# Performance work log

Measured on AMD Instinct MI355X. Metric: run time of the kernel, lower is better.

## Reference

```python
import jax, jax.numpy as jnp
import numpy as np

NS, NA = 50000, 50000
ES, EA = 1000000, 500000
XD, UD, HD, MH = 8, 8, 64, 64


def _mlp_params(key, d_in, d_h, d_out):
    ks = jax.random.split(key, 3)
    s = 0.05
    return (jax.random.normal(ks[0], (d_in, d_h), jnp.float32) * s, jnp.zeros((d_h,), jnp.float32),
            jax.random.normal(ks[1], (d_h, d_h), jnp.float32) * s, jnp.zeros((d_h,), jnp.float32),
            jax.random.normal(ks[2], (d_h, d_out), jnp.float32) * s, jnp.zeros((d_out,), jnp.float32))


def _mlp(z, w1, b1, w2, b2, w3, b3):
    z = jnp.tanh(z @ w1 + b1)
    z = jnp.tanh(z @ w2 + b2)
    return z @ w3 + b3


def setup_inputs() -> dict:
    key = jax.random.key(0)
    ks = jax.random.split(key, 12)
    inp = {
        'pos_state': jax.random.uniform(ks[0], (NS, 2), jnp.float32),
        'pos_action': jax.random.uniform(ks[1], (NA, 2), jnp.float32),
        'h': jax.random.normal(ks[2], (NS, HD), jnp.float32),
        'x': jax.random.normal(ks[3], (NS, XD), jnp.float32),
        'u': jax.random.normal(ks[4], (NA, UD), jnp.float32),
        'a2s_src': jax.random.randint(ks[5], (EA,), 0, NA, jnp.int32),
        'a2s_dst': jax.random.randint(ks[6], (EA,), 0, NS, jnp.int32),
        'a2s_dis': jax.random.uniform(ks[7], (EA, 1), jnp.float32),
        's2s_src': jax.random.randint(ks[8], (ES,), 0, NS, jnp.int32),
        's2s_dst': jax.random.randint(ks[9], (ES,), 0, NS, jnp.int32),
        's2s_dis': jax.random.uniform(ks[10], (ES, 1), jnp.float32),
    }
    pk = jax.random.split(ks[11], 3)
    u2h = _mlp_params(pk[0], 2 * 2 + 1 + UD, MH, HD)
    x2h = _mlp_params(pk[1], 2 * 2 + 1 + XD + HD, MH, HD)
    upd = _mlp_params(pk[2], 2 + 3 * HD + XD, MH, HD)
    for pref, p in (('u2h', u2h), ('x2h', x2h), ('upd', upd)):
        for i, (w, b) in enumerate(zip(p[0::2], p[1::2]), 1):
            inp[f'{pref}_w{i}'] = w
            inp[f'{pref}_b{i}'] = b
    return inp


def reference(pos_state, pos_action, h, x, u,
              a2s_src, a2s_dst, a2s_dis, s2s_src, s2s_dst, s2s_dis,
              u2h_w1, u2h_b1, u2h_w2, u2h_b2, u2h_w3, u2h_b3,
              x2h_w1, x2h_b1, x2h_w2, x2h_b2, x2h_w3, x2h_b3,
              upd_w1, upd_b1, upd_w2, upd_b2, upd_w3, upd_b3):
    ns = pos_state.shape[0]
    # a2s: gather action src / state dst, per-edge MLP, sum into dst state nodes
    msg_u_in = jnp.concatenate([pos_action[a2s_src], pos_state[a2s_dst], a2s_dis, u[a2s_src]], axis=-1)
    msg_u = _mlp(msg_u_in, u2h_w1, u2h_b1, u2h_w2, u2h_b2, u2h_w3, u2h_b3)  # [EA, HD]
    sum_u = jax.ops.segment_sum(msg_u, a2s_dst, num_segments=ns)
    # s2s: gather state src/dst, per-edge MLP, mean into dst state nodes
    msg_x_in = jnp.concatenate([pos_state[s2s_src], pos_state[s2s_dst], s2s_dis, x[s2s_src], h[s2s_src]], axis=-1)
    msg_x = _mlp(msg_x_in, x2h_w1, x2h_b1, x2h_w2, x2h_b2, x2h_w3, x2h_b3)  # [ES, HD]
    sum_x = jax.ops.segment_sum(msg_x, s2s_dst, num_segments=ns)
    deg = jax.ops.segment_sum(jnp.ones((s2s_dst.shape[0],), jnp.float32), s2s_dst, num_segments=ns)
    mean_x = sum_x / jnp.maximum(deg, 1.0)[:, None]  # DGL mean: 0 for zero in-degree
    # node update MLP
    upd_in = jnp.concatenate([pos_state, h, sum_u, mean_x, x], axis=-1)
    return _mlp(upd_in, upd_w1, upd_b1, upd_w2, upd_b2, upd_w3, upd_b3)
```

## Files before the change

kernel.cpp:

```cpp
#include <hip/hip_runtime.h>
#include <hip/hip_bf16.h>


typedef __attribute__((ext_vector_type(8))) short short8;
typedef __attribute__((ext_vector_type(4))) float f32x4;

#define MFMA(a, b, c) __builtin_amdgcn_mfma_f32_16x16x32_bf16(a, b, c, 0, 0, 0)

union FU { short8 v; unsigned int d[4]; unsigned short us[8]; };

__device__ __forceinline__ unsigned short f2bf(float f) {
    unsigned u = __float_as_uint(f);
    u += 0x7fffu + ((u >> 16) & 1u);
    return (unsigned short)(u >> 16);
}
__device__ __forceinline__ unsigned int pack2(float a, float b) {
    return (unsigned int)f2bf(a) | ((unsigned int)f2bf(b) << 16);
}
__device__ __forceinline__ unsigned int pk2(float a, float b) {
    float2 t; t.x = a; t.y = b;
    union { __hip_bfloat162 h; unsigned int u; } c;
    c.h = __float22bfloat162_rn(t);
    return c.u;
}
__device__ __forceinline__ float tanh_fast(float xv) {
    float t = __builtin_amdgcn_exp2f(xv * 2.8853900817779268f);
    return 1.0f - 2.0f * __builtin_amdgcn_rcpf(t + 1.0f);
}

template <typename KM>
__device__ void build_gfrags(const float* __restrict__ w, unsigned short* dst,
                             int nchunks, int gtid, int gstr, KM km) {
    int total = nchunks * 4 * 64;
    for (int f = gtid; f < total; f += gstr) {
        int lv = f & 63, nt = (f >> 6) & 3, c = f >> 8;
        int n = nt * 16 + (lv & 15);
        int kb = c * 32 + ((lv >> 4) << 3);
        unsigned short* o = dst + f * 8;
        #pragma unroll
        for (int j = 0; j < 8; ++j) {
            int sk = km(kb + j);
            o[j] = (sk >= 0) ? f2bf(w[sk * 64 + n]) : (unsigned short)0;
        }
    }
}

#define PERM_KM [](int k) -> int { return (k >> 2) + 16 * (k & 3); }

__global__ __launch_bounds__(256) void build_wtab(
    const float* __restrict__ s_w1, const float* __restrict__ s_w2, const float* __restrict__ s_w3,
    const float* __restrict__ a_w1, const float* __restrict__ a_w2, const float* __restrict__ a_w3,
    const float* __restrict__ u_w1, const float* __restrict__ u_w2, const float* __restrict__ u_w3,
    unsigned short* __restrict__ ts, unsigned short* __restrict__ ta,
    unsigned short* __restrict__ tu)
{
    int gtid = blockIdx.x * 256 + threadIdx.x;
    int gstr = gridDim.x * 256;
    build_gfrags(s_w1, ts, 3, gtid, gstr, [](int k) -> int {
        if (k < 2)   return k;
        if (k < 74)  return k + 3;
        if (k < 80)  return -2;
        if (k < 82)  return k - 78;
        if (k == 82) return 4;
        return -2; });
    build_gfrags(s_w2, ts + 3 * 2048, 2, gtid, gstr, PERM_KM);
    build_gfrags(s_w3, ts + 5 * 2048, 2, gtid, gstr, PERM_KM);
    build_gfrags(a_w1, ta, 1, gtid, gstr, [](int k) -> int {
        if (k < 2)   return k;
        if (k < 10)  return k + 3;
        if (k < 16)  return -2;
        if (k < 18)  return k - 14;
        if (k == 18) return 4;
        return -2; });
    build_gfrags(a_w2, ta + 1 * 2048, 2, gtid, gstr, PERM_KM);
    build_gfrags(a_w3, ta + 3 * 2048, 2, gtid, gstr, PERM_KM);
    build_gfrags(u_w1, tu, 7, gtid, gstr, [](int k) -> int {
        return (k < 202) ? k : -2; });
    build_gfrags(u_w2, tu + 7 * 2048, 2, gtid, gstr, PERM_KM);
    build_gfrags(u_w3, tu + 9 * 2048, 2, gtid, gstr, PERM_KM);
}

#define ZTRANS(Zw, accv)                                                       \
    _Pragma("unroll")                                                          \
    for (int r = 0; r < 4; ++r) {                                              \
        uint2 pv;                                                              \
        pv.x = pk2(tanh_fast(accv[0][r]), tanh_fast(accv[1][r]));              \
        pv.y = pk2(tanh_fast(accv[2][r]), tanh_fast(accv[3][r]));              \
        *(uint2*)((Zw) + ((q << 2) + r) * 72 + (m16 << 2)) = pv;               \
    }

__global__ __launch_bounds__(256) void prep1(
    const float* __restrict__ ps, const float* __restrict__ pa,
    const float* __restrict__ h, const float* __restrict__ x,
    const float* __restrict__ u,
    const int* __restrict__ s2s_dst, const int* __restrict__ a2s_dst,
    unsigned short* __restrict__ s_row, unsigned short* __restrict__ a_row,
    int* __restrict__ cnt_s, int* __restrict__ rank_s,
    int* __restrict__ cnt_a, int* __restrict__ rank_a,
    int NS, int NA, int ES, int EA)
{
    int R0 = NS * 80, R1 = R0 + NA * 16, R2 = R1 + ES, R3 = R2 + EA;
    for (int i = blockIdx.x * 256 + threadIdx.x; i < R3; i += gridDim.x * 256) {
        if (i < R0) {
            int n = i / 80, k = i - n * 80;
            float v = (k < 2) ? ps[n * 2 + k] : (k < 10) ? x[n * 8 + k - 2]
                    : (k < 74) ? h[n * 64 + k - 10] : 0.f;
            s_row[i] = f2bf(v);
        } else if (i < R1) {
            int j = i - R0; int a = j / 16, k = j - a * 16;
            float v = (k < 2) ? pa[a * 2 + k] : (k < 10) ? u[a * 8 + k - 2] : 0.f;
            a_row[j] = f2bf(v);
        } else if (i < R2) {
            int e = i - R1;
            rank_s[e] = atomicAdd(&cnt_s[s2s_dst[e]], 1);
        } else {
            int e = i - R2;
            rank_a[e] = atomicAdd(&cnt_a[a2s_dst[e]], 1);
        }
    }
}

#define SCAN_CHUNK 1024

__global__ __launch_bounds__(256) void scan_a(const int* __restrict__ cnt,
                                              int* __restrict__ bsum, int N2)
{
    __shared__ int red[256];
    int t = threadIdx.x;
    int base = blockIdx.x * SCAN_CHUNK + t * 4;
    int s = 0;
    #pragma unroll
    for (int j = 0; j < 4; ++j) { int i = base + j; if (i < N2) s += cnt[i]; }
    red[t] = s; __syncthreads();
    for (int d = 128; d > 0; d >>= 1) {
        if (t < d) red[t] += red[t + d];
        __syncthreads();
    }
    if (t == 0) bsum[blockIdx.x] = red[0];
}

__global__ __launch_bounds__(128) void scan_b(int* __restrict__ bsum, int NB)
{
    __shared__ int part[128];
    int t = threadIdx.x;
    int v = (t < NB) ? bsum[t] : 0;
    part[t] = v; __syncthreads();
    for (int d = 1; d < 128; d <<= 1) {
        int w = (t >= d) ? part[t - d] : 0;
        __syncthreads();
        part[t] += w;
        __syncthreads();
    }
    if (t < NB) bsum[t] = part[t] - v;
}

__global__ __launch_bounds__(256) void scan_c(const int* __restrict__ cnt,
                                              const int* __restrict__ bsum,
                                              int* __restrict__ off,
                                              int N2, int NS, int ES)
{
    __shared__ int part[256];
    int t = threadIdx.x;
    int base = blockIdx.x * SCAN_CHUNK + t * 4;
    int c[4]; int s = 0;
    #pragma unroll
    for (int j = 0; j < 4; ++j) { int i = base + j; c[j] = (i < N2) ? cnt[i] : 0; s += c[j]; }
    part[t] = s; __syncthreads();
    for (int d = 1; d < 256; d <<= 1) {
        int w = (t >= d) ? part[t - d] : 0;
        __syncthreads();
        part[t] += w;
        __syncthreads();
    }
    int run = bsum[blockIdx.x] + part[t] - s;
    #pragma unroll
    for (int j = 0; j < 4; ++j) {
        int i = base + j;
        if (i < N2) off[i] = run - ((i >= NS) ? ES : 0);
        run += c[j];
    }
}

__global__ __launch_bounds__(256) void scatter_sort2(
    const int* __restrict__ srcS, const int* __restrict__ dstS,
    const int* __restrict__ rankS, const int* __restrict__ offS,
    const float* __restrict__ disS,
    const int* __restrict__ srcA, const int* __restrict__ dstA,
    const int* __restrict__ rankA, const int* __restrict__ offA,
    const float* __restrict__ disA,
    const float* __restrict__ ps,
    int* __restrict__ ssrcS, int* __restrict__ sdstS, unsigned short* __restrict__ spadS,
    int* __restrict__ ssrcA, int* __restrict__ sdstA, unsigned short* __restrict__ spadA,
    int ES, int EA)
{
    int tot = ES + EA;
    for (int i = blockIdx.x * 256 + threadIdx.x; i < tot; i += gridDim.x * 256) {
        if (i < ES) {
            int d = dstS[i];
            int pos = offS[d] + rankS[i];
            ssrcS[pos] = srcS[i];
            sdstS[pos] = d;
            uint2 p;
            p.x = pack2(ps[d * 2], ps[d * 2 + 1]);
            p.y = (unsigned)f2bf(disS[i]) | (0x3F80u << 16);
            *(uint2*)(spadS + (size_t)pos * 4) = p;
        } else {
            int e = i - ES;
            int d = dstA[e];
            int pos = offA[d] + rankA[e];
            ssrcA[pos] = srcA[e];
            sdstA[pos] = d;
            uint2 p;
            p.x = pack2(ps[d * 2], ps[d * 2 + 1]);
            p.y = (unsigned)f2bf(disA[e]) | (0x3F80u << 16);
            *(uint2*)(spadA + (size_t)pos * 4) = p;
        }
    }
}

__global__ __launch_bounds__(256) void s2s_mfma(
    const unsigned short* __restrict__ s_row,
    const int* __restrict__ ssrc, const int* __restrict__ sdst,
    const unsigned short* __restrict__ spad,
    const unsigned short* __restrict__ wtab,
    const float* __restrict__ b1, const float* __restrict__ b2,
    const float* __restrict__ b3,
    float* __restrict__ sum_x, int E)
{
    __shared__ __align__(16) unsigned short WT[7 * 2048];
    __shared__ __align__(16) unsigned short Z[4][16 * 72];

    int tid = threadIdx.x;
    for (int i = tid * 8; i < 7 * 2048; i += 256 * 8)
        *(short8*)(WT + i) = *(const short8*)(wtab + i);
    __syncthreads();

    const unsigned short* W1 = WT;
    const unsigned short* W2 = WT + 3 * 2048;
    const unsigned short* W3 = WT + 5 * 2048;

    int wid = tid >> 6, lane = tid & 63, m16 = lane & 15, q = lane >> 4;
    unsigned short* Zw = Z[wid];

    float bb1[4], bb2[4], bb3[4];
    #pragma unroll
    for (int nt = 0; nt < 4; ++nt) {
        bb1[nt] = b1[nt * 16 + m16];
        bb2[nt] = b2[nt * 16 + m16];
        bb3[nt] = b3[nt * 16 + m16];
    }

    int T = E >> 5;
    for (int t = blockIdx.x * 4 + wid; t < T; t += gridDim.x * 4) {
        int p0 = t * 32;
        int sp0 = p0 + ((m16 >> 2) << 3) + (m16 & 3);
        int sp1 = sp0 + 4;
        int s0 = ssrc[sp0], s1 = ssrc[sp1];
        int pb = p0 + (q << 3);
        int4 dq0 = *(const int4*)(sdst + pb);
        int4 dq1 = *(const int4*)(sdst + pb + 4);
        int dseq[8] = {dq0.x, dq0.y, dq0.z, dq0.w, dq1.x, dq1.y, dq1.z, dq1.w};

        FU Lb[2][3]; uint2 ep[2];
        const unsigned short* rA = s_row + (size_t)s0 * 80;
        const unsigned short* rB = s_row + (size_t)s1 * 80;
        #pragma unroll
        for (int c = 0; c < 3; ++c) {
            Lb[0][c].v = *(const short8*)(rA + c * 32 + q * 8);
            Lb[1][c].v = *(const short8*)(rB + c * 32 + q * 8);
        }
        ep[0] = *(const uint2*)(spad + (size_t)sp0 * 4);
        ep[1] = *(const uint2*)(spad + (size_t)sp1 * 4);
        #pragma unroll
        for (int mt = 0; mt < 2; ++mt) {
            FU f = Lb[mt][2];
            f.d[0] = q < 2 ? f.d[0] : (q == 2 ? ep[mt].x : 0u);
            f.d[1] = q < 2 ? f.d[1] : (q == 2 ? ep[mt].y : 0u);
            f.d[2] = q < 2 ? f.d[2] : 0u;
            f.d[3] = q < 2 ? f.d[3] : 0u;
            Lb[mt][2] = f;
        }

        f32x4 acc1[2][4];
        #pragma unroll
        for (int mt = 0; mt < 2; ++mt)
            #pragma unroll
            for (int nt = 0; nt < 4; ++nt)
                acc1[mt][nt] = (f32x4){bb1[nt], bb1[nt], bb1[nt], bb1[nt]};
        #pragma unroll
        for (int c = 0; c < 3; ++c)
            #pragma unroll
            for (int nt = 0; nt < 4; ++nt) {
                short8 wf = *(const short8*)(W1 + ((c * 4 + nt) * 64 + lane) * 8);
                acc1[0][nt] = MFMA(Lb[0][c].v, wf, acc1[0][nt]);
                acc1[1][nt] = MFMA(Lb[1][c].v, wf, acc1[1][nt]);
            }

        f32x4 a3[2][4];
        #pragma unroll
        for (int mt = 0; mt < 2; ++mt) {
            ZTRANS(Zw, acc1[mt])
            FU A2[2];
            A2[0].v = *(const short8*)(Zw + m16 * 72 + 0 * 32 + q * 8);
            A2[1].v = *(const short8*)(Zw + m16 * 72 + 1 * 32 + q * 8);

            f32x4 a2[4];
            #pragma unroll
            for (int nt = 0; nt < 4; ++nt) {
                a2[nt] = (f32x4){bb2[nt], bb2[nt], bb2[nt], bb2[nt]};
                short8 w0 = *(const short8*)(W2 + ((0 * 4 + nt) * 64 + lane) * 8);
                short8 w1f = *(const short8*)(W2 + ((1 * 4 + nt) * 64 + lane) * 8);
                a2[nt] = MFMA(A2[0].v, w0, a2[nt]);
                a2[nt] = MFMA(A2[1].v, w1f, a2[nt]);
            }

            ZTRANS(Zw, a2)
            FU A3[2];
            A3[0].v = *(const short8*)(Zw + m16 * 72 + 0 * 32 + q * 8);
            A3[1].v = *(const short8*)(Zw + m16 * 72 + 1 * 32 + q * 8);

            #pragma unroll
            for (int nt = 0; nt < 4; ++nt) {
                a3[mt][nt] = (f32x4){bb3[nt], bb3[nt], bb3[nt], bb3[nt]};
                short8 w0 = *(const short8*)(W3 + ((0 * 4 + nt) * 64 + lane) * 8);
                short8 w1f = *(const short8*)(W3 + ((1 * 4 + nt) * 64 + lane) * 8);
                a3[mt][nt] = MFMA(A3[0].v, w0, a3[mt][nt]);
                a3[mt][nt] = MFMA(A3[1].v, w1f, a3[mt][nt]);
            }
        }

        #pragma unroll
        for (int j = 0; j < 8; ++j) {
            int mt = j >> 2, r = j & 3;
            bool merge = (j < 7) && (dseq[j] == dseq[j + 1]);
            if (merge) {
                int mt2 = (j + 1) >> 2, r2 = (j + 1) & 3;
                #pragma unroll
                for (int nt = 0; nt < 4; ++nt) a3[mt2][nt][r2] += a3[mt][nt][r];
            } else {
                float* pbase = sum_x + (size_t)dseq[j] * 64 + m16;
                #pragma unroll
                for (int nt = 0; nt < 4; ++nt)
                    unsafeAtomicAdd(pbase + nt * 16, a3[mt][nt][r]);
            }
        }
    }
}

__global__ __launch_bounds__(256) void a2s_mfma(
    const unsigned short* __restrict__ a_row,
    const int* __restrict__ ssrc, const int* __restrict__ sdst,
    const unsigned short* __restrict__ spad,
    const unsigned short* __restrict__ wtab,
    const float* __restrict__ b1, const float* __restrict__ b2,
    const float* __restrict__ b3,
    float* __restrict__ sum_u, int E)
{
    __shared__ __align__(16) unsigned short WT[5 * 2048];
    __shared__ __align__(16) unsigned short Z[4][16 * 72];

    int tid = threadIdx.x;
    for (int i = tid * 8; i < 5 * 2048; i += 256 * 8)
        *(short8*)(WT + i) = *(const short8*)(wtab + i);
    __syncthreads();

    const unsigned short* W1 = WT;
    const unsigned short* W2 = WT + 1 * 2048;
    const unsigned short* W3 = WT + 3 * 2048;

    int wid = tid >> 6, lane = tid & 63, m16 = lane & 15, q = lane >> 4;
    unsigned short* Zw = Z[wid];

    float bb1[4], bb2[4], bb3[4];
    #pragma unroll
    for (int nt = 0; nt < 4; ++nt) {
        bb1[nt] = b1[nt * 16 + m16];
        bb2[nt] = b2[nt * 16 + m16];
        bb3[nt] = b3[nt * 16 + m16];
    }

    int T = E >> 5;
    for (int t = blockIdx.x * 4 + wid; t < T; t += gridDim.x * 4) {
        int p0 = t * 32;
        int sp0 = p0 + ((m16 >> 2) << 3) + (m16 & 3);
        int sp1 = sp0 + 4;
        int s0 = ssrc[sp0], s1 = ssrc[sp1];
        int pb = p0 + (q << 3);
        int4 dq0 = *(const int4*)(sdst + pb);
        int4 dq1 = *(const int4*)(sdst + pb + 4);
        int dseq[8] = {dq0.x, dq0.y, dq0.z, dq0.w, dq1.x, dq1.y, dq1.z, dq1.w};

        FU Lb[2]; uint2 ep[2];
        Lb[0].v = *(const short8*)(a_row + (size_t)s0 * 16 + q * 8);
        Lb[1].v = *(const short8*)(a_row + (size_t)s1 * 16 + q * 8);
        ep[0] = *(const uint2*)(spad + (size_t)sp0 * 4);
        ep[1] = *(const uint2*)(spad + (size_t)sp1 * 4);
        #pragma unroll
        for (int mt = 0; mt < 2; ++mt) {
            FU f = Lb[mt];
            f.d[0] = q < 2 ? f.d[0] : (q == 2 ? ep[mt].x : 0u);
            f.d[1] = q < 2 ? f.d[1] : (q == 2 ? ep[mt].y : 0u);
            f.d[2] = q < 2 ? f.d[2] : 0u;
            f.d[3] = q < 2 ? f.d[3] : 0u;
            Lb[mt] = f;
        }

        f32x4 acc1[2][4];
        #pragma unroll
        for (int mt = 0; mt < 2; ++mt)
            #pragma unroll
            for (int nt = 0; nt < 4; ++nt)
                acc1[mt][nt] = (f32x4){bb1[nt], bb1[nt], bb1[nt], bb1[nt]};
        #pragma unroll
        for (int nt = 0; nt < 4; ++nt) {
            short8 wf = *(const short8*)(W1 + (nt * 64 + lane) * 8);
            acc1[0][nt] = MFMA(Lb[0].v, wf, acc1[0][nt]);
            acc1[1][nt] = MFMA(Lb[1].v, wf, acc1[1][nt]);
        }

        f32x4 a3[2][4];
        #pragma unroll
        for (int mt = 0; mt < 2; ++mt) {
            ZTRANS(Zw, acc1[mt])
            FU A2[2];
            A2[0].v = *(const short8*)(Zw + m16 * 72 + 0 * 32 + q * 8);
            A2[1].v = *(const short8*)(Zw + m16 * 72 + 1 * 32 + q * 8);

            f32x4 a2[4];
            #pragma unroll
            for (int nt = 0; nt < 4; ++nt) {
                a2[nt] = (f32x4){bb2[nt], bb2[nt], bb2[nt], bb2[nt]};
                short8 w0 = *(const short8*)(W2 + ((0 * 4 + nt) * 64 + lane) * 8);
                short8 w1f = *(const short8*)(W2 + ((1 * 4 + nt) * 64 + lane) * 8);
                a2[nt] = MFMA(A2[0].v, w0, a2[nt]);
                a2[nt] = MFMA(A2[1].v, w1f, a2[nt]);
            }

            ZTRANS(Zw, a2)
            FU A3[2];
            A3[0].v = *(const short8*)(Zw + m16 * 72 + 0 * 32 + q * 8);
            A3[1].v = *(const short8*)(Zw + m16 * 72 + 1 * 32 + q * 8);

            #pragma unroll
            for (int nt = 0; nt < 4; ++nt) {
                a3[mt][nt] = (f32x4){bb3[nt], bb3[nt], bb3[nt], bb3[nt]};
                short8 w0 = *(const short8*)(W3 + ((0 * 4 + nt) * 64 + lane) * 8);
                short8 w1f = *(const short8*)(W3 + ((1 * 4 + nt) * 64 + lane) * 8);
                a3[mt][nt] = MFMA(A3[0].v, w0, a3[mt][nt]);
                a3[mt][nt] = MFMA(A3[1].v, w1f, a3[mt][nt]);
            }
        }

        #pragma unroll
        for (int j = 0; j < 8; ++j) {
            int mt = j >> 2, r = j & 3;
            bool merge = (j < 7) && (dseq[j] == dseq[j + 1]);
            if (merge) {
                int mt2 = (j + 1) >> 2, r2 = (j + 1) & 3;
                #pragma unroll
                for (int nt = 0; nt < 4; ++nt) a3[mt2][nt][r2] += a3[mt][nt][r];
            } else {
                float* pbase = sum_u + (size_t)dseq[j] * 64 + m16;
                #pragma unroll
                for (int nt = 0; nt < 4; ++nt)
                    unsafeAtomicAdd(pbase + nt * 16, a3[mt][nt][r]);
            }
        }
    }
}

__global__ __launch_bounds__(256) void prep2(
    const float* __restrict__ ps, const float* __restrict__ h,
    const float* __restrict__ x,
    const float* __restrict__ su, const float* __restrict__ sx,
    const int* __restrict__ cnt_s, unsigned short* __restrict__ u_row, int NS)
{
    int n = blockIdx.x;
    int k = threadIdx.x;
    if (k >= 224) return;
    float v;
    if (k < 2)        v = ps[n * 2 + k];
    else if (k < 66)  v = h[n * 64 + k - 2];
    else if (k < 130) v = su[n * 64 + k - 66];
    else if (k < 194) v = sx[n * 64 + k - 130] * (1.0f / fmaxf((float)cnt_s[n], 1.0f));
    else if (k < 202) v = x[n * 8 + k - 194];
    else              v = 0.f;
    u_row[(size_t)n * 224 + k] = f2bf(v);
}

__global__ __launch_bounds__(256) void upd_mfma(
    const unsigned short* __restrict__ u_row,
    const unsigned short* __restrict__ wtab,
    const float* __restrict__ b1, const float* __restrict__ b2,
    const float* __restrict__ b3,
    float* __restrict__ out, int NS)
{
    __shared__ __align__(16) unsigned short WT[11 * 2048];
    __shared__ __align__(16) unsigned short Z[4][16 * 72];

    int tid = threadIdx.x;
    for (int i = tid * 8; i < 11 * 2048; i += 256 * 8)
        *(short8*)(WT + i) = *(const short8*)(wtab + i);
    __syncthreads();

    const unsigned short* W1 = WT;
    const unsigned short* W2 = WT + 7 * 2048;
    const unsigned short* W3 = WT + 9 * 2048;

    int wid = tid >> 6, lane = tid & 63, m16 = lane & 15, q = lane >> 4;
    unsigned short* Zw = Z[wid];

    float bb1[4], bb2[4], bb3[4];
    #pragma unroll
    for (int nt = 0; nt < 4; ++nt) {
        bb1[nt] = b1[nt * 16 + m16];
        bb2[nt] = b2[nt * 16 + m16];
        bb3[nt] = b3[nt * 16 + m16];
    }

    int T = NS >> 4;
    for (int t = blockIdx.x * 4 + wid; t < T; t += gridDim.x * 4) {
        int n0 = t * 16;
        const unsigned short* row = u_row + (size_t)(n0 + m16) * 224;

        f32x4 acc1[4];
        #pragma unroll
        for (int nt = 0; nt < 4; ++nt)
            acc1[nt] = (f32x4){bb1[nt], bb1[nt], bb1[nt], bb1[nt]};
        #pragma unroll
        for (int c = 0; c < 7; ++c) {
            short8 afrag = *(const short8*)(row + c * 32 + q * 8);
            #pragma unroll
            for (int nt = 0; nt < 4; ++nt) {
                short8 wf = *(const short8*)(W1 + ((c * 4 + nt) * 64 + lane) * 8);
                acc1[nt] = MFMA(afrag, wf, acc1[nt]);
            }
        }

        ZTRANS(Zw, acc1)
        FU A2[2];
        A2[0].v = *(const short8*)(Zw + m16 * 72 + 0 * 32 + q * 8);
        A2[1].v = *(const short8*)(Zw + m16 * 72 + 1 * 32 + q * 8);

        f32x4 a2[4];
        #pragma unroll
        for (int nt = 0; nt < 4; ++nt) {
            a2[nt] = (f32x4){bb2[nt], bb2[nt], bb2[nt], bb2[nt]};
            short8 w0 = *(const short8*)(W2 + ((0 * 4 + nt) * 64 + lane) * 8);
            short8 w1f = *(const short8*)(W2 + ((1 * 4 + nt) * 64 + lane) * 8);
            a2[nt] = MFMA(A2[0].v, w0, a2[nt]);
            a2[nt] = MFMA(A2[1].v, w1f, a2[nt]);
        }

        ZTRANS(Zw, a2)
        FU A3[2];
        A3[0].v = *(const short8*)(Zw + m16 * 72 + 0 * 32 + q * 8);
        A3[1].v = *(const short8*)(Zw + m16 * 72 + 1 * 32 + q * 8);

        f32x4 a3[4];
        #pragma unroll
        for (int nt = 0; nt < 4; ++nt) {
            a3[nt] = (f32x4){bb3[nt], bb3[nt], bb3[nt], bb3[nt]};
            short8 w0 = *(const short8*)(W3 + ((0 * 4 + nt) * 64 + lane) * 8);
            short8 w1f = *(const short8*)(W3 + ((1 * 4 + nt) * 64 + lane) * 8);
            a3[nt] = MFMA(A3[0].v, w0, a3[nt]);
            a3[nt] = MFMA(A3[1].v, w1f, a3[nt]);
        }

        #pragma unroll
        for (int nt = 0; nt < 4; ++nt)
            #pragma unroll
            for (int r = 0; r < 4; ++r)
                out[(size_t)(n0 + (q << 2) + r) * 64 + nt * 16 + m16] = a3[nt][r];
    }
}

extern "C" void kernel_launch(void* const* d_in, const int* in_sizes, int n_in,
                              void* d_out, int out_size, void* d_ws, size_t ws_size,
                              hipStream_t stream) {
    const float* pos_state  = (const float*)d_in[0];
    const float* pos_action = (const float*)d_in[1];
    const float* h          = (const float*)d_in[2];
    const float* x          = (const float*)d_in[3];
    const float* u          = (const float*)d_in[4];
    const int*   a2s_src    = (const int*)d_in[5];
    const int*   a2s_dst    = (const int*)d_in[6];
    const float* a2s_dis    = (const float*)d_in[7];
    const int*   s2s_src    = (const int*)d_in[8];
    const int*   s2s_dst    = (const int*)d_in[9];
    const float* s2s_dis    = (const float*)d_in[10];
    const float* u2h_w1 = (const float*)d_in[11]; const float* u2h_b1 = (const float*)d_in[12];
    const float* u2h_w2 = (const float*)d_in[13]; const float* u2h_b2 = (const float*)d_in[14];
    const float* u2h_w3 = (const float*)d_in[15]; const float* u2h_b3 = (const float*)d_in[16];
    const float* x2h_w1 = (const float*)d_in[17]; const float* x2h_b1 = (const float*)d_in[18];
    const float* x2h_w2 = (const float*)d_in[19]; const float* x2h_b2 = (const float*)d_in[20];
    const float* x2h_w3 = (const float*)d_in[21]; const float* x2h_b3 = (const float*)d_in[22];
    const float* upd_w1 = (const float*)d_in[23]; const float* upd_b1 = (const float*)d_in[24];
    const float* upd_w2 = (const float*)d_in[25]; const float* upd_b2 = (const float*)d_in[26];
    const float* upd_w3 = (const float*)d_in[27]; const float* upd_b3 = (const float*)d_in[28];

    int NS = in_sizes[0] / 2;
    int NA = in_sizes[1] / 2;
    int EA = in_sizes[5];
    int ES = in_sizes[8];
    int N2 = 2 * NS;
    int NB = (N2 + SCAN_CHUNK - 1) / SCAN_CHUNK;

    char* p = (char*)d_ws;
    int*   cnt2  = (int*)p;            p += (size_t)N2 * 4;
    float* sum_u = (float*)p;          p += (size_t)NS * 64 * 4;
    float* sum_x = (float*)p;          p += (size_t)NS * 64 * 4;
    size_t zbytes = (size_t)(p - (char*)d_ws);
    unsigned short* u_row = (unsigned short*)p;
    int*   off2   = (int*)p;           p += (size_t)N2 * 4;
    int*   rank_s = (int*)p;           p += (size_t)ES * 4;
    int*   rank_a = (int*)p;           p += (size_t)EA * 4;
    int*   ssrc_s = (int*)p;           p += (size_t)ES * 4;
    int*   sdst_s = (int*)p;           p += (size_t)ES * 4;
    unsigned short* spad_s = (unsigned short*)p; p += (size_t)ES * 8;
    int*   ssrc_a = (int*)p;           p += (size_t)EA * 4;
    int*   sdst_a = (int*)p;           p += (size_t)EA * 4;
    unsigned short* spad_a = (unsigned short*)p; p += (size_t)EA * 8;
    unsigned short* s_row  = (unsigned short*)p; p += (size_t)NS * 80 * 2;
    unsigned short* a_row  = (unsigned short*)p; p += (size_t)NA * 16 * 2;
    int*   bsum   = (int*)p;           p += 128 * 4;
    unsigned short* wtab_s = (unsigned short*)p; p += 7 * 2048 * 2;
    unsigned short* wtab_a = (unsigned short*)p; p += 5 * 2048 * 2;
    unsigned short* wtab_u = (unsigned short*)p; p += 11 * 2048 * 2;
    (void)ws_size;

    int* cnt_s = cnt2;
    int* cnt_a = cnt2 + NS;
    int* off_s = off2;
    int* off_a = off2 + NS;

    hipMemsetAsync(d_ws, 0, zbytes, stream);

    build_wtab<<<24, 256, 0, stream>>>(x2h_w1, x2h_w2, x2h_w3,
                                       u2h_w1, u2h_w2, u2h_w3,
                                       upd_w1, upd_w2, upd_w3,
                                       wtab_s, wtab_a, wtab_u);
    prep1<<<2048, 256, 0, stream>>>(pos_state, pos_action, h, x, u,
                                    s2s_dst, a2s_dst,
                                    s_row, a_row,
                                    cnt_s, rank_s, cnt_a, rank_a,
                                    NS, NA, ES, EA);
    scan_a<<<NB, 256, 0, stream>>>(cnt2, bsum, N2);
    scan_b<<<1, 128, 0, stream>>>(bsum, NB);
    scan_c<<<NB, 256, 0, stream>>>(cnt2, bsum, off2, N2, NS, ES);
    scatter_sort2<<<1024, 256, 0, stream>>>(s2s_src, s2s_dst, rank_s, off_s, s2s_dis,
                                            a2s_src, a2s_dst, rank_a, off_a, a2s_dis,
                                            pos_state,
                                            ssrc_s, sdst_s, spad_s,
                                            ssrc_a, sdst_a, spad_a, ES, EA);
    a2s_mfma<<<1024, 256, 0, stream>>>(a_row, ssrc_a, sdst_a, spad_a, wtab_a,
                                       u2h_b1, u2h_b2, u2h_b3, sum_u, EA);
    s2s_mfma<<<1024, 256, 0, stream>>>(s_row, ssrc_s, sdst_s, spad_s, wtab_s,
                                       x2h_b1, x2h_b2, x2h_b3, sum_x, ES);
    prep2<<<NS, 256, 0, stream>>>(pos_state, h, x, sum_u, sum_x, cnt_s, u_row, NS);
    upd_mfma<<<784, 256, 0, stream>>>(u_row, wtab_u,
                                      upd_b1, upd_b2, upd_b3,
                                      (float*)d_out, NS);
}
```

Measured before the change: 508.8 us.

## Fuse weight prep into prep1, merge edge kernels, fold prep2 into upd

Folds the weight-fragment build into extra blocks of prep1, merges the a2s and s2s edge MLP kernels into one launch split by block index, and removes prep2 by having upd_mfma read h, sums and x directly in fp32 and convert to bf16 in registers. The scatter stage now stores the raw fp32 distance instead of a packed bf16 pad, and the edge kernel gathers dst positions itself. Fewer launches and one less full intermediate buffer round-trip, at the cost of extra gathers inside the edge kernel and a reordered upd weight layout.

```diff
diff --git a/kernel.cpp b/kernel.cpp
--- a/kernel.cpp
+++ b/kernel.cpp
@@ -13,9 +13,6 @@
     unsigned u = __float_as_uint(f);
     u += 0x7fffu + ((u >> 16) & 1u);
     return (unsigned short)(u >> 16);
-}
-__device__ __forceinline__ unsigned int pack2(float a, float b) {
-    return (unsigned int)f2bf(a) | ((unsigned int)f2bf(b) << 16);
 }
 __device__ __forceinline__ unsigned int pk2(float a, float b) {
     float2 t; t.x = a; t.y = b;
@@ -47,39 +44,6 @@
 
 #define PERM_KM [](int k) -> int { return (k >> 2) + 16 * (k & 3); }
 
-__global__ __launch_bounds__(256) void build_wtab(
-    const float* __restrict__ s_w1, const float* __restrict__ s_w2, const float* __restrict__ s_w3,
-    const float* __restrict__ a_w1, const float* __restrict__ a_w2, const float* __restrict__ a_w3,
-    const float* __restrict__ u_w1, const float* __restrict__ u_w2, const float* __restrict__ u_w3,
-    unsigned short* __restrict__ ts, unsigned short* __restrict__ ta,
-    unsigned short* __restrict__ tu)
-{
-    int gtid = blockIdx.x * 256 + threadIdx.x;
-    int gstr = gridDim.x * 256;
-    build_gfrags(s_w1, ts, 3, gtid, gstr, [](int k) -> int {
-        if (k < 2)   return k;
-        if (k < 74)  return k + 3;
-        if (k < 80)  return -2;
-        if (k < 82)  return k - 78;
-        if (k == 82) return 4;
-        return -2; });
-    build_gfrags(s_w2, ts + 3 * 2048, 2, gtid, gstr, PERM_KM);
-    build_gfrags(s_w3, ts + 5 * 2048, 2, gtid, gstr, PERM_KM);
-    build_gfrags(a_w1, ta, 1, gtid, gstr, [](int k) -> int {
-        if (k < 2)   return k;
-        if (k < 10)  return k + 3;
-        if (k < 16)  return -2;
-        if (k < 18)  return k - 14;
-        if (k == 18) return 4;
-        return -2; });
-    build_gfrags(a_w2, ta + 1 * 2048, 2, gtid, gstr, PERM_KM);
-    build_gfrags(a_w3, ta + 3 * 2048, 2, gtid, gstr, PERM_KM);
-    build_gfrags(u_w1, tu, 7, gtid, gstr, [](int k) -> int {
-        return (k < 202) ? k : -2; });
-    build_gfrags(u_w2, tu + 7 * 2048, 2, gtid, gstr, PERM_KM);
-    build_gfrags(u_w3, tu + 9 * 2048, 2, gtid, gstr, PERM_KM);
-}
-
 #define ZTRANS(Zw, accv)                                                       \
     _Pragma("unroll")                                                          \
     for (int r = 0; r < 4; ++r) {                                              \
@@ -97,10 +61,47 @@
     unsigned short* __restrict__ s_row, unsigned short* __restrict__ a_row,
     int* __restrict__ cnt_s, int* __restrict__ rank_s,
     int* __restrict__ cnt_a, int* __restrict__ rank_a,
-    int NS, int NA, int ES, int EA)
-{
+    const float* __restrict__ s_w1, const float* __restrict__ s_w2, const float* __restrict__ s_w3,
+    const float* __restrict__ a_w1, const float* __restrict__ a_w2, const float* __restrict__ a_w3,
+    const float* __restrict__ u_w1, const float* __restrict__ u_w2, const float* __restrict__ u_w3,
+    unsigned short* __restrict__ ts, unsigned short* __restrict__ ta,
+    unsigned short* __restrict__ tu,
+    int NS, int NA, int ES, int EA, int MAINB)
+{
+    int bid = blockIdx.x;
+    if (bid >= MAINB) {
+        int gtid = (bid - MAINB) * 256 + threadIdx.x;
+        int gstr = (gridDim.x - MAINB) * 256;
+        build_gfrags(s_w1, ts, 3, gtid, gstr, [](int k) -> int {
+            if (k < 2)   return k;
+            if (k < 74)  return k + 3;
+            if (k < 80)  return -2;
+            if (k < 82)  return k - 78;
+            if (k == 82) return 4;
+            return -2; });
+        build_gfrags(s_w2, ts + 3 * 2048, 2, gtid, gstr, PERM_KM);
+        build_gfrags(s_w3, ts + 5 * 2048, 2, gtid, gstr, PERM_KM);
+        build_gfrags(a_w1, ta, 1, gtid, gstr, [](int k) -> int {
+            if (k < 2)   return k;
+            if (k < 10)  return k + 3;
+            if (k < 16)  return -2;
+            if (k < 18)  return k - 14;
+            if (k == 18) return 4;
+            return -2; });
+        build_gfrags(a_w2, ta + 1 * 2048, 2, gtid, gstr, PERM_KM);
+        build_gfrags(a_w3, ta + 3 * 2048, 2, gtid, gstr, PERM_KM);
+        build_gfrags(u_w1, tu, 7, gtid, gstr, [](int k) -> int {
+            if (k < 192) return k + 2;
+            if (k < 194) return k - 192;
+            if (k < 202) return k;
+            return -2; });
+        build_gfrags(u_w2, tu + 7 * 2048, 2, gtid, gstr, PERM_KM);
+        build_gfrags(u_w3, tu + 9 * 2048, 2, gtid, gstr, PERM_KM);
+        return;
+    }
+
     int R0 = NS * 80, R1 = R0 + NA * 16, R2 = R1 + ES, R3 = R2 + EA;
-    for (int i = blockIdx.x * 256 + threadIdx.x; i < R3; i += gridDim.x * 256) {
+    for (int i = bid * 256 + threadIdx.x; i < R3; i += MAINB * 256) {
         if (i < R0) {
             int n = i / 80, k = i - n * 80;
             float v = (k < 2) ? ps[n * 2 + k] : (k < 10) ? x[n * 8 + k - 2]
@@ -188,9 +189,8 @@
     const int* __restrict__ srcA, const int* __restrict__ dstA,
     const int* __restrict__ rankA, const int* __restrict__ offA,
     const float* __restrict__ disA,
-    const float* __restrict__ ps,
-    int* __restrict__ ssrcS, int* __restrict__ sdstS, unsigned short* __restrict__ spadS,
-    int* __restrict__ ssrcA, int* __restrict__ sdstA, unsigned short* __restrict__ spadA,
+    int* __restrict__ ssrcS, int* __restrict__ sdstS, float* __restrict__ sdisS,
+    int* __restrict__ ssrcA, int* __restrict__ sdstA, float* __restrict__ sdisA,
     int ES, int EA)
 {
     int tot = ES + EA;
@@ -200,47 +200,35 @@
             int pos = offS[d] + rankS[i];
             ssrcS[pos] = srcS[i];
             sdstS[pos] = d;
-            uint2 p;
-            p.x = pack2(ps[d * 2], ps[d * 2 + 1]);
-            p.y = (unsigned)f2bf(disS[i]) | (0x3F80u << 16);
-            *(uint2*)(spadS + (size_t)pos * 4) = p;
+            sdisS[pos] = disS[i];
         } else {
             int e = i - ES;
             int d = dstA[e];
             int pos = offA[d] + rankA[e];
             ssrcA[pos] = srcA[e];
             sdstA[pos] = d;
-            uint2 p;
-            p.x = pack2(ps[d * 2], ps[d * 2 + 1]);
-            p.y = (unsigned)f2bf(disA[e]) | (0x3F80u << 16);
-            *(uint2*)(spadA + (size_t)pos * 4) = p;
-        }
-    }
-}
-
-__global__ __launch_bounds__(256) void s2s_mfma(
-    const unsigned short* __restrict__ s_row,
+            sdisA[pos] = disA[e];
+        }
+    }
+}
+
+template <int C1, int RS>
+__device__ __forceinline__ void edge_path(
+    const unsigned short* __restrict__ row_tab,
     const int* __restrict__ ssrc, const int* __restrict__ sdst,
-    const unsigned short* __restrict__ spad,
-    const unsigned short* __restrict__ wtab,
+    const float* __restrict__ sdis, const float* __restrict__ ps,
+    const unsigned short* WT,
     const float* __restrict__ b1, const float* __restrict__ b2,
     const float* __restrict__ b3,
-    float* __restrict__ sum_x, int E)
-{
-    __shared__ __align__(16) unsigned short WT[7 * 2048];
-    __shared__ __align__(16) unsigned short Z[4][16 * 72];
-
-    int tid = threadIdx.x;
-    for (int i = tid * 8; i < 7 * 2048; i += 256 * 8)
-        *(short8*)(WT + i) = *(const short8*)(wtab + i);
-    __syncthreads();
-
+    float* __restrict__ sums, int E, int bid0, int nb, int tid,
+    unsigned short* Zbase)
+{
     const unsigned short* W1 = WT;
-    const unsigned short* W2 = WT + 3 * 2048;
-    const unsigned short* W3 = WT + 5 * 2048;
+    const unsigned short* W2 = WT + C1 * 2048;
+    const unsigned short* W3 = WT + (C1 + 2) * 2048;
 
     int wid = tid >> 6, lane = tid & 63, m16 = lane & 15, q = lane >> 4;
-    unsigned short* Zw = Z[wid];
+    unsigned short* Zw = Zbase + wid * (16 * 72);
 
     float bb1[4], bb2[4], bb3[4];
     #pragma unroll
@@ -251,7 +239,7 @@
     }
 
     int T = E >> 5;
-    for (int t = blockIdx.x * 4 + wid; t < T; t += gridDim.x * 4) {
+    for (int t = bid0 * 4 + wid; t < T; t += nb * 4) {
         int p0 = t * 32;
         int sp0 = p0 + ((m16 >> 2) << 3) + (m16 & 3);
         int sp1 = sp0 + 4;
@@ -261,24 +249,31 @@
         int4 dq1 = *(const int4*)(sdst + pb + 4);
         int dseq[8] = {dq0.x, dq0.y, dq0.z, dq0.w, dq1.x, dq1.y, dq1.z, dq1.w};
 
-        FU Lb[2][3]; uint2 ep[2];
-        const unsigned short* rA = s_row + (size_t)s0 * 80;
-        const unsigned short* rB = s_row + (size_t)s1 * 80;
-        #pragma unroll
-        for (int c = 0; c < 3; ++c) {
-            Lb[0][c].v = *(const short8*)(rA + c * 32 + q * 8);
-            Lb[1][c].v = *(const short8*)(rB + c * 32 + q * 8);
-        }
-        ep[0] = *(const uint2*)(spad + (size_t)sp0 * 4);
-        ep[1] = *(const uint2*)(spad + (size_t)sp1 * 4);
-        #pragma unroll
-        for (int mt = 0; mt < 2; ++mt) {
-            FU f = Lb[mt][2];
-            f.d[0] = q < 2 ? f.d[0] : (q == 2 ? ep[mt].x : 0u);
-            f.d[1] = q < 2 ? f.d[1] : (q == 2 ? ep[mt].y : 0u);
-            f.d[2] = q < 2 ? f.d[2] : 0u;
-            f.d[3] = q < 2 ? f.d[3] : 0u;
-            Lb[mt][2] = f;
+        uint2 ep[2];
+        ep[0].x = 0; ep[0].y = 0; ep[1].x = 0; ep[1].y = 0;
+        if (q == 2) {
+            int dA = sdst[sp0], dB = sdst[sp1];
+            float2 pA = *(const float2*)(ps + 2 * dA);
+            float2 pB = *(const float2*)(ps + 2 * dB);
+            float zA = sdis[sp0], zB = sdis[sp1];
+            ep[0].x = pk2(pA.x, pA.y); ep[0].y = (unsigned)f2bf(zA) | (0x3F80u << 16);
+            ep[1].x = pk2(pB.x, pB.y); ep[1].y = (unsigned)f2bf(zB) | (0x3F80u << 16);
+        }
+
+        FU Lb[2][C1];
+        const unsigned short* rA = row_tab + (size_t)s0 * RS;
+        const unsigned short* rB = row_tab + (size_t)s1 * RS;
+        #pragma unroll
+        for (int c = 0; c < C1; ++c) {
+            int off = c * 32 + q * 8;
+            bool valid = (c < C1 - 1) || (q < 2);
+            if (valid) {
+                Lb[0][c].v = *(const short8*)(rA + off);
+                Lb[1][c].v = *(const short8*)(rB + off);
+            } else {
+                Lb[0][c].d[0] = ep[0].x; Lb[0][c].d[1] = ep[0].y; Lb[0][c].d[2] = 0; Lb[0][c].d[3] = 0;
+                Lb[1][c].d[0] = ep[1].x; Lb[1][c].d[1] = ep[1].y; Lb[1][c].d[2] = 0; Lb[1][c].d[3] = 0;
+            }
         }
 
         f32x4 acc1[2][4];
@@ -288,7 +283,7 @@
             for (int nt = 0; nt < 4; ++nt)
                 acc1[mt][nt] = (f32x4){bb1[nt], bb1[nt], bb1[nt], bb1[nt]};
         #pragma unroll
-        for (int c = 0; c < 3; ++c)
+        for (int c = 0; c < C1; ++c)
             #pragma unroll
             for (int nt = 0; nt < 4; ++nt) {
                 short8 wf = *(const short8*)(W1 + ((c * 4 + nt) * 64 + lane) * 8);
@@ -338,7 +333,7 @@
                 #pragma unroll
                 for (int nt = 0; nt < 4; ++nt) a3[mt2][nt][r2] += a3[mt][nt][r];
             } else {
-                float* pbase = sum_x + (size_t)dseq[j] * 64 + m16;
+                float* pbase = sums + (size_t)dseq[j] * 64 + m16;
                 #pragma unroll
                 for (int nt = 0; nt < 4; ++nt)
                     unsafeAtomicAdd(pbase + nt * 16, a3[mt][nt][r]);
@@ -347,29 +342,60 @@
     }
 }
 
-__global__ __launch_bounds__(256) void a2s_mfma(
-    const unsigned short* __restrict__ a_row,
-    const int* __restrict__ ssrc, const int* __restrict__ sdst,
-    const unsigned short* __restrict__ spad,
+__global__ __launch_bounds__(256) void edges_mfma(
+    const unsigned short* __restrict__ s_row, const unsigned short* __restrict__ a_row,
+    const int* __restrict__ ssS, const int* __restrict__ sdS, const float* __restrict__ szS,
+    const int* __restrict__ ssA, const int* __restrict__ sdA, const float* __restrict__ szA,
+    const unsigned short* __restrict__ wtS, const unsigned short* __restrict__ wtA,
+    const float* __restrict__ sb1, const float* __restrict__ sb2, const float* __restrict__ sb3,
+    const float* __restrict__ ab1, const float* __restrict__ ab2, const float* __restrict__ ab3,
+    const float* __restrict__ ps,
+    float* __restrict__ sum_x, float* __restrict__ sum_u,
+    int ES, int EA, int SPLIT)
+{
+    __shared__ __align__(16) unsigned short WT[7 * 2048];
+    __shared__ __align__(16) unsigned short Z[4][16 * 72];
+
+    int tid = threadIdx.x, bid = blockIdx.x;
+    bool is_s = bid < SPLIT;
+    const unsigned short* wt = is_s ? wtS : wtA;
+    int wtn = is_s ? 7 * 2048 : 5 * 2048;
+    for (int i = tid * 8; i < wtn; i += 256 * 8)
+        *(short8*)(WT + i) = *(const short8*)(wt + i);
+    __syncthreads();
+
+    if (is_s)
+        edge_path<3, 80>(s_row, ssS, sdS, szS, ps, WT, sb1, sb2, sb3,
+                         sum_x, ES, bid, SPLIT, tid, &Z[0][0]);
+    else
+        edge_path<1, 16>(a_row, ssA, sdA, szA, ps, WT, ab1, ab2, ab3,
+                         sum_u, EA, bid - SPLIT, gridDim.x - SPLIT, tid, &Z[0][0]);
+}
+
+__global__ __launch_bounds__(256) void upd_mfma(
+    const float* __restrict__ ps, const float* __restrict__ h,
+    const float* __restrict__ x,
+    const float* __restrict__ su, const float* __restrict__ sx,
+    const int* __restrict__ cnt_s,
     const unsigned short* __restrict__ wtab,
     const float* __restrict__ b1, const float* __restrict__ b2,
     const float* __restrict__ b3,
-    float* __restrict__ sum_u, int E)
-{
-    __shared__ __align__(16) unsigned short WT[5 * 2048];
+    float* __restrict__ out, int NS)
+{
+    __shared__ __align__(16) unsigned short WT[11 * 2048];
     __shared__ __align__(16) unsigned short Z[4][16 * 72];
 
     int tid = threadIdx.x;
-    for (int i = tid * 8; i < 5 * 2048; i += 256 * 8)
+    for (int i = tid * 8; i < 11 * 2048; i += 256 * 8)
         *(short8*)(WT + i) = *(const short8*)(wtab + i);
     __syncthreads();
 
     const unsigned short* W1 = WT;
-    const unsigned short* W2 = WT + 1 * 2048;
-    const unsigned short* W3 = WT + 3 * 2048;
+    const unsigned short* W2 = WT + 7 * 2048;
+    const unsigned short* W3 = WT + 9 * 2048;
 
     int wid = tid >> 6, lane = tid & 63, m16 = lane & 15, q = lane >> 4;
-    unsigned short* Zw = Z[wid];
+    unsigned short* Zw = &Z[wid][0];
 
     float bb1[4], bb2[4], bb3[4];
     #pragma unroll
@@ -379,163 +405,54 @@
         bb3[nt] = b3[nt * 16 + m16];
     }
 
-    int T = E >> 5;
-    for (int t = blockIdx.x * 4 + wid; t < T; t += gridDim.x * 4) {
-        int p0 = t * 32;
-        int sp0 = p0 + ((m16 >> 2) << 3) + (m16 & 3);
-        int sp1 = sp0 + 4;
-        int s0 = ssrc[sp0], s1 = ssrc[sp1];
-        int pb = p0 + (q << 3);
-        int4 dq0 = *(const int4*)(sdst + pb);
-        int4 dq1 = *(const int4*)(sdst + pb + 4);
-        int dseq[8] = {dq0.x, dq0.y, dq0.z, dq0.w, dq1.x, dq1.y, dq1.z, dq1.w};
-
-        FU Lb[2]; uint2 ep[2];
-        Lb[0].v = *(const short8*)(a_row + (size_t)s0 * 16 + q * 8);
-        Lb[1].v = *(const short8*)(a_row + (size_t)s1 * 16 + q * 8);
-        ep[0] = *(const uint2*)(spad + (size_t)sp0 * 4);
-        ep[1] = *(const uint2*)(spad + (size_t)sp1 * 4);
-        #pragma unroll
-        for (int mt = 0; mt < 2; ++mt) {
-            FU f = Lb[mt];
-            f.d[0] = q < 2 ? f.d[0] : (q == 2 ? ep[mt].x : 0u);
-            f.d[1] = q < 2 ? f.d[1] : (q == 2 ? ep[mt].y : 0u);
-            f.d[2] = q < 2 ? f.d[2] : 0u;
-            f.d[3] = q < 2 ? f.d[3] : 0u;
-            Lb[mt] = f;
-        }
-
-        f32x4 acc1[2][4];
-        #pragma unroll
-        for (int mt = 0; mt < 2; ++mt)
-            #pragma unroll
-            for (int nt = 0; nt < 4; ++nt)
-                acc1[mt][nt] = (f32x4){bb1[nt], bb1[nt], bb1[nt], bb1[nt]};
-        #pragma unroll
-        for (int nt = 0; nt < 4; ++nt) {
-            short8 wf = *(const short8*)(W1 + (nt * 64 + lane) * 8);
-            acc1[0][nt] = MFMA(Lb[0].v, wf, acc1[0][nt]);
-            acc1[1][nt] = MFMA(Lb[1].v, wf, acc1[1][nt]);
-        }
-
-        f32x4 a3[2][4];
-        #pragma unroll
-        for (int mt = 0; mt < 2; ++mt) {
-            ZTRANS(Zw, acc1[mt])
-            FU A2[2];
-            A2[0].v = *(const short8*)(Zw + m16 * 72 + 0 * 32 + q * 8);
-            A2[1].v = *(const short8*)(Zw + m16 * 72 + 1 * 32 + q * 8);
-
-            f32x4 a2[4];
-            #pragma unroll
-            for (int nt = 0; nt < 4; ++nt) {
-                a2[nt] = (f32x4){bb2[nt], bb2[nt], bb2[nt], bb2[nt]};
-                short8 w0 = *(const short8*)(W2 + ((0 * 4 + nt) * 64 + lane) * 8);
-                short8 w1f = *(const short8*)(W2 + ((1 * 4 + nt) * 64 + lane) * 8);
-                a2[nt] = MFMA(A2[0].v, w0, a2[nt]);
-                a2[nt] = MFMA(A2[1].v, w1f, a2[nt]);
-            }
-
-            ZTRANS(Zw, a2)
-            FU A3[2];
-            A3[0].v = *(const short8*)(Zw + m16 * 72 + 0 * 32 + q * 8);
-            A3[1].v = *(const short8*)(Zw + m16 * 72 + 1 * 32 + q * 8);
-
-            #pragma unroll
-            for (int nt = 0; nt < 4; ++nt) {
-                a3[mt][nt] = (f32x4){bb3[nt], bb3[nt], bb3[nt], bb3[nt]};
-                short8 w0 = *(const short8*)(W3 + ((0 * 4 + nt) * 64 + lane) * 8);
-                short8 w1f = *(const short8*)(W3 + ((1 * 4 + nt) * 64 + lane) * 8);
-                a3[mt][nt] = MFMA(A3[0].v, w0, a3[mt][nt]);
-                a3[mt][nt] = MFMA(A3[1].v, w1f, a3[mt][nt]);
-            }
-        }
-
-        #pragma unroll
-        for (int j = 0; j < 8; ++j) {
-            int mt = j >> 2, r = j & 3;
-            bool merge = (j < 7) && (dseq[j] == dseq[j + 1]);
-            if (merge) {
-                int mt2 = (j + 1) >> 2, r2 = (j + 1) & 3;
-                #pragma unroll
-                for (int nt = 0; nt < 4; ++nt) a3[mt2][nt][r2] += a3[mt][nt][r];
-            } else {
-                float* pbase = sum_u + (size_t)dseq[j] * 64 + m16;
-                #pragma unroll
-                for (int nt = 0; nt < 4; ++nt)
-                    unsafeAtomicAdd(pbase + nt * 16, a3[mt][nt][r]);
-            }
-        }
-    }
-}
-
-__global__ __launch_bounds__(256) void prep2(
-    const float* __restrict__ ps, const float* __restrict__ h,
-    const float* __restrict__ x,
-    const float* __restrict__ su, const float* __restrict__ sx,
-    const int* __restrict__ cnt_s, unsigned short* __restrict__ u_row, int NS)
-{
-    int n = blockIdx.x;
-    int k = threadIdx.x;
-    if (k >= 224) return;
-    float v;
-    if (k < 2)        v = ps[n * 2 + k];
-    else if (k < 66)  v = h[n * 64 + k - 2];
-    else if (k < 130) v = su[n * 64 + k - 66];
-    else if (k < 194) v = sx[n * 64 + k - 130] * (1.0f / fmaxf((float)cnt_s[n], 1.0f));
-    else if (k < 202) v = x[n * 8 + k - 194];
-    else              v = 0.f;
-    u_row[(size_t)n * 224 + k] = f2bf(v);
-}
-
-__global__ __launch_bounds__(256) void upd_mfma(
-    const unsigned short* __restrict__ u_row,
-    const unsigned short* __restrict__ wtab,
-    const float* __restrict__ b1, const float* __restrict__ b2,
-    const float* __restrict__ b3,
-    float* __restrict__ out, int NS)
-{
-    __shared__ __align__(16) unsigned short WT[11 * 2048];
-    __shared__ __align__(16) unsigned short Z[4][16 * 72];
-
-    int tid = threadIdx.x;
-    for (int i = tid * 8; i < 11 * 2048; i += 256 * 8)
-        *(short8*)(WT + i) = *(const short8*)(wtab + i);
-    __syncthreads();
-
-    const unsigned short* W1 = WT;
-    const unsigned short* W2 = WT + 7 * 2048;
-    const unsigned short* W3 = WT + 9 * 2048;
-
-    int wid = tid >> 6, lane = tid & 63, m16 = lane & 15, q = lane >> 4;
-    unsigned short* Zw = Z[wid];
-
-    float bb1[4], bb2[4], bb3[4];
-    #pragma unroll
-    for (int nt = 0; nt < 4; ++nt) {
-        bb1[nt] = b1[nt * 16 + m16];
-        bb2[nt] = b2[nt * 16 + m16];
-        bb3[nt] = b3[nt * 16 + m16];
-    }
-
     int T = NS >> 4;
     for (int t = blockIdx.x * 4 + wid; t < T; t += gridDim.x * 4) {
         int n0 = t * 16;
-        const unsigned short* row = u_row + (size_t)(n0 + m16) * 224;
+        int n = n0 + m16;
+        float rd = __builtin_amdgcn_rcpf(fmaxf((float)cnt_s[n], 1.0f));
+
+        FU A[7];
+        const float* hp = h + (size_t)n * 64;
+        const float* sup = su + (size_t)n * 64;
+        const float* sxp = sx + (size_t)n * 64;
+        #pragma unroll
+        for (int c = 0; c < 6; ++c) {
+            const float* src = (c < 2) ? hp : (c < 4) ? sup : sxp;
+            int base = (c & 1) * 32 + q * 8;
+            float4 f0 = *(const float4*)(src + base);
+            float4 f1 = *(const float4*)(src + base + 4);
+            if (c >= 4) {
+                f0.x *= rd; f0.y *= rd; f0.z *= rd; f0.w *= rd;
+                f1.x *= rd; f1.y *= rd; f1.z *= rd; f1.w *= rd;
+            }
+            A[c].d[0] = pk2(f0.x, f0.y); A[c].d[1] = pk2(f0.z, f0.w);
+            A[c].d[2] = pk2(f1.x, f1.y); A[c].d[3] = pk2(f1.z, f1.w);
+        }
+        A[6].d[0] = 0; A[6].d[1] = 0; A[6].d[2] = 0; A[6].d[3] = 0;
+        if (q == 0) {
+            float2 pp = *(const float2*)(ps + 2 * n);
+            float4 x0 = *(const float4*)(x + 8 * n);
+            float2 x1 = *(const float2*)(x + 8 * n + 4);
+            A[6].d[0] = pk2(pp.x, pp.y);
+            A[6].d[1] = pk2(x0.x, x0.y);
+            A[6].d[2] = pk2(x0.z, x0.w);
+            A[6].d[3] = pk2(x1.x, x1.y);
+        } else if (q == 1) {
+            float2 x2 = *(const float2*)(x + 8 * n + 6);
+            A[6].d[0] = pk2(x2.x, x2.y);
+        }
 
         f32x4 acc1[4];
         #pragma unroll
         for (int nt = 0; nt < 4; ++nt)
             acc1[nt] = (f32x4){bb1[nt], bb1[nt], bb1[nt], bb1[nt]};
         #pragma unroll
-        for (int c = 0; c < 7; ++c) {
-            short8 afrag = *(const short8*)(row + c * 32 + q * 8);
+        for (int c = 0; c < 7; ++c)
             #pragma unroll
             for (int nt = 0; nt < 4; ++nt) {
                 short8 wf = *(const short8*)(W1 + ((c * 4 + nt) * 64 + lane) * 8);
-                acc1[nt] = MFMA(afrag, wf, acc1[nt]);
-            }
-        }
+                acc1[nt] = MFMA(A[c].v, wf, acc1[nt]);
+            }
 
         ZTRANS(Zw, acc1)
         FU A2[2];
@@ -611,16 +528,15 @@
     float* sum_u = (float*)p;          p += (size_t)NS * 64 * 4;
     float* sum_x = (float*)p;          p += (size_t)NS * 64 * 4;
     size_t zbytes = (size_t)(p - (char*)d_ws);
-    unsigned short* u_row = (unsigned short*)p;
     int*   off2   = (int*)p;           p += (size_t)N2 * 4;
     int*   rank_s = (int*)p;           p += (size_t)ES * 4;
     int*   rank_a = (int*)p;           p += (size_t)EA * 4;
     int*   ssrc_s = (int*)p;           p += (size_t)ES * 4;
     int*   sdst_s = (int*)p;           p += (size_t)ES * 4;
-    unsigned short* spad_s = (unsigned short*)p; p += (size_t)ES * 8;
+    float* sdis_s = (float*)p;         p += (size_t)ES * 4;
     int*   ssrc_a = (int*)p;           p += (size_t)EA * 4;
     int*   sdst_a = (int*)p;           p += (size_t)EA * 4;
-    unsigned short* spad_a = (unsigned short*)p; p += (size_t)EA * 8;
+    float* sdis_a = (float*)p;         p += (size_t)EA * 4;
     unsigned short* s_row  = (unsigned short*)p; p += (size_t)NS * 80 * 2;
     unsigned short* a_row  = (unsigned short*)p; p += (size_t)NA * 16 * 2;
     int*   bsum   = (int*)p;           p += 128 * 4;
@@ -636,29 +552,31 @@
 
     hipMemsetAsync(d_ws, 0, zbytes, stream);
 
-    build_wtab<<<24, 256, 0, stream>>>(x2h_w1, x2h_w2, x2h_w3,
-                                       u2h_w1, u2h_w2, u2h_w3,
-                                       upd_w1, upd_w2, upd_w3,
-                                       wtab_s, wtab_a, wtab_u);
-    prep1<<<2048, 256, 0, stream>>>(pos_state, pos_action, h, x, u,
-                                    s2s_dst, a2s_dst,
-                                    s_row, a_row,
-                                    cnt_s, rank_s, cnt_a, rank_a,
-                                    NS, NA, ES, EA);
+    const int MAINB = 2048;
+    prep1<<<MAINB + 24, 256, 0, stream>>>(pos_state, pos_action, h, x, u,
+                                          s2s_dst, a2s_dst, s_row, a_row,
+                                          cnt_s, rank_s, cnt_a, rank_a,
+                                          x2h_w1, x2h_w2, x2h_w3,
+                                          u2h_w1, u2h_w2, u2h_w3,
+                                          upd_w1, upd_w2, upd_w3,
+                                          wtab_s, wtab_a, wtab_u,
+                                          NS, NA, ES, EA, MAINB);
     scan_a<<<NB, 256, 0, stream>>>(cnt2, bsum, N2);
     scan_b<<<1, 128, 0, stream>>>(bsum, NB);
     scan_c<<<NB, 256, 0, stream>>>(cnt2, bsum, off2, N2, NS, ES);
     scatter_sort2<<<1024, 256, 0, stream>>>(s2s_src, s2s_dst, rank_s, off_s, s2s_dis,
                                             a2s_src, a2s_dst, rank_a, off_a, a2s_dis,
-                                            pos_state,
-                                            ssrc_s, sdst_s, spad_s,
-                                            ssrc_a, sdst_a, spad_a, ES, EA);
-    a2s_mfma<<<1024, 256, 0, stream>>>(a_row, ssrc_a, sdst_a, spad_a, wtab_a,
-                                       u2h_b1, u2h_b2, u2h_b3, sum_u, EA);
-    s2s_mfma<<<1024, 256, 0, stream>>>(s_row, ssrc_s, sdst_s, spad_s, wtab_s,
-                                       x2h_b1, x2h_b2, x2h_b3, sum_x, ES);
-    prep2<<<NS, 256, 0, stream>>>(pos_state, h, x, sum_u, sum_x, cnt_s, u_row, NS);
-    upd_mfma<<<784, 256, 0, stream>>>(u_row, wtab_u,
-                                      upd_b1, upd_b2, upd_b3,
+                                            ssrc_s, sdst_s, sdis_s,
+                                            ssrc_a, sdst_a, sdis_a, ES, EA);
+    edges_mfma<<<1536, 256, 0, stream>>>(s_row, a_row,
+                                         ssrc_s, sdst_s, sdis_s,
+                                         ssrc_a, sdst_a, sdis_a,
+                                         wtab_s, wtab_a,
+                                         x2h_b1, x2h_b2, x2h_b3,
+                                         u2h_b1, u2h_b2, u2h_b3,
+                                         pos_state, sum_x, sum_u,
+                                         ES, EA, 1024);
+    upd_mfma<<<784, 256, 0, stream>>>(pos_state, h, x, sum_u, sum_x, cnt_s,
+                                      wtab_u, upd_b1, upd_b2, upd_b3,
                                       (float*)d_out, NS);
 }
```

Result: faster. 445.9 us (-12.4%).
